# Performance work log

Measured on AMD Instinct MI355X. Metric: run time of the kernel, lower is better.

The kernel has to match this reference:

```python
import jax, jax.numpy as jnp
import numpy as np

N = 1_000_000   # voxels (stride-1: in grid == out grid)
C = 32          # channels
K = 27          # 3x3x3 kernel offsets
P = 600_000     # rulebook pairs per offset
BN_EPS = 1e-5


def setup_inputs() -> dict:
    key = jax.random.key(0)
    k1, k2, k3, k4 = jax.random.split(key, 4)
    x = jax.random.normal(k1, (N, C), dtype=jnp.float32)
    # He-style init for conv weights: fan_in = K * C
    W = jax.random.normal(k2, (K, C, C), dtype=jnp.float32) * (1.0 / np.sqrt(K * C))
    gamma = jnp.ones((C,), dtype=jnp.float32)
    beta = jnp.zeros((C,), dtype=jnp.float32)
    in_idx = jax.random.randint(k3, (K, P), 0, N, dtype=jnp.int32)
    out_idx = jax.random.randint(k4, (K, P), 0, N, dtype=jnp.int32)
    return {"x": x, "W": W, "gamma": gamma, "beta": beta,
            "in_idx": in_idx, "out_idx": out_idx}


def _sparse_conv(x, W, in_idx, out_idx):
    # Rulebook-driven sparse conv: for each kernel offset k, gather input
    # voxels, multiply by the offset's [C,C] weight, scatter-add to outputs.
    def step(acc, inputs):
        ii, oi, w = inputs                      # [P], [P], [C,C]
        acc = acc.at[oi].add(x[ii] @ w)          # gather -> GEMM -> scatter
        return acc, None
    out0 = jnp.zeros((x.shape[0], W.shape[-1]), dtype=x.dtype)
    out, _ = jax.lax.scan(step, out0, (in_idx, out_idx, W))
    return out


def reference(x, W, gamma, beta, in_idx, out_idx):
    y = _sparse_conv(x, W, in_idx, out_idx)      # [N, C]
    # BatchNorm (training-mode batch stats over all voxels, per channel)
    mean = jnp.mean(y, axis=0)
    var = jnp.var(y, axis=0)
    y = (y - mean) * jax.lax.rsqrt(var + BN_EPS) * gamma + beta
    # ReLU
    return jnp.maximum(y, 0.0)
```

## Files before the change

### kernel.cpp

```cpp
#include <hip/hip_runtime.h>

#define CH 32
#define KOFF 27
#define BN_EPS 1e-5f
#define FXS 512.0f
#define FXI (1.0f / 512.0f)

typedef short bf16x8 __attribute__((ext_vector_type(8)));
typedef float f32x4 __attribute__((ext_vector_type(4)));
typedef unsigned long long u64;

__device__ __forceinline__ unsigned short f2bf(float f) {
    unsigned u = __builtin_bit_cast(unsigned, f);
    u = (u + 0x7fffu + ((u >> 16) & 1u)) >> 16;
    return (unsigned short)u;
}

__device__ __forceinline__ void decode4(u64 v, float* f) {
    long long w = (long long)v;
    int s0 = (short)(w & 0xFFFF);          w -= (long long)s0;
    int s1 = (short)((w >> 16) & 0xFFFF);  w -= ((long long)s1 << 16);
    int s2 = (short)((w >> 32) & 0xFFFF);  w -= ((long long)s2 << 32);
    int s3 = (int)(w >> 48);
    f[0] = s0 * FXI; f[1] = s1 * FXI; f[2] = s2 * FXI; f[3] = s3 * FXI;
}

__global__ __launch_bounds__(256) void conv_fx_kernel(
    const float* __restrict__ x, const float* __restrict__ W,
    const int* __restrict__ in_idx, const int* __restrict__ out_idx,
    u64* __restrict__ yfx,
    int P, int tilesPerK, int tilesPerWave)
{
    const int k    = blockIdx.y;
    const int lane = threadIdx.x & 63;
    const int wv   = threadIdx.x >> 6;
    const int r16  = lane & 15;
    const int g    = lane >> 4;

    const float* Wk = W + k * CH * CH;
    bf16x8 b0, b1;
#pragma unroll
    for (int j = 0; j < 8; ++j) {
        int kk = g * 8 + j;
        b0[j] = (short)f2bf(Wk[kk * CH + 2 * r16]);
        b1[j] = (short)f2bf(Wk[kk * CH + 2 * r16 + 1]);
    }

    const int kP = k * P;
    int t0 = (blockIdx.x * 4 + wv) * tilesPerWave;
    int t1 = t0 + tilesPerWave;
    if (t1 > tilesPerK) t1 = tilesPerK;

    const int iBase = (r16 & 1) ? 2 : 0;
    const int m     = r16 >> 1;

    for (int t = t0; t < t1; ++t) {
        const int base = t * 16;
        int pi = base + r16;
        if (pi >= P) pi = P - 1;
        const int ii = in_idx[kP + pi];
        const float* xr = x + ii * CH + g * 8;
        f32x4 x0 = *(const f32x4*)xr;
        f32x4 x1 = *(const f32x4*)(xr + 4);
        bf16x8 a;
        a[0] = (short)f2bf(x0[0]); a[1] = (short)f2bf(x0[1]);
        a[2] = (short)f2bf(x0[2]); a[3] = (short)f2bf(x0[3]);
        a[4] = (short)f2bf(x1[0]); a[5] = (short)f2bf(x1[1]);
        a[6] = (short)f2bf(x1[2]); a[7] = (short)f2bf(x1[3]);

        f32x4 d0 = {0.f, 0.f, 0.f, 0.f};
        f32x4 d1 = {0.f, 0.f, 0.f, 0.f};
        d0 = __builtin_amdgcn_mfma_f32_16x16x32_bf16(a, b0, d0, 0, 0, 0);
        d1 = __builtin_amdgcn_mfma_f32_16x16x32_bf16(a, b1, d1, 0, 0, 0);

        unsigned qi[4];
#pragma unroll
        for (int i = 0; i < 4; ++i) {
            int s0 = __float2int_rn(d0[i] * FXS);
            int s1 = __float2int_rn(d1[i] * FXS);
            qi[i] = (unsigned)(s0 & 0xFFFF) | ((unsigned)s1 << 16);
        }
        unsigned pq[4];
#pragma unroll
        for (int i = 0; i < 4; ++i) pq[i] = (unsigned)__shfl_xor((int)qi[i], 1);

#pragma unroll
        for (int s = 0; s < 2; ++s) {
            const int i  = iBase + s;
            const int pr = base + g * 4 + i;
            if (pr < P) {
                const int oi = out_idx[kP + pr];
                int a0 = (short)(qi[i] & 0xFFFF), a1 = (short)(qi[i] >> 16);
                int c0 = (short)(pq[i] & 0xFFFF), c1 = (short)(pq[i] >> 16);
                long long A;
                if (!(r16 & 1))
                    A = (long long)a0 + ((long long)a1 << 16)
                      + ((long long)c0 << 32) + ((long long)c1 << 48);
                else
                    A = (long long)c0 + ((long long)c1 << 16)
                      + ((long long)a0 << 32) + ((long long)a1 << 48);
                atomicAdd(&yfx[(size_t)oi * 8 + m], (u64)A);
            }
        }
    }
}

__global__ __launch_bounds__(256) void stats_fx_kernel(
    const u64* __restrict__ yfx, float* __restrict__ stats, int nW)
{
    __shared__ float ls[CH], ls2[CH];
    if (threadIdx.x < CH) { ls[threadIdx.x] = 0.f; ls2[threadIdx.x] = 0.f; }
    __syncthreads();

    int tid = blockIdx.x * blockDim.x + threadIdx.x;
    int stride = gridDim.x * blockDim.x;
    float s[4] = {0,0,0,0}, q[4] = {0,0,0,0};
    for (int i = tid; i < nW; i += stride) {
        float f[4];
        decode4(yfx[i], f);
#pragma unroll
        for (int j = 0; j < 4; ++j) { s[j] += f[j]; q[j] += f[j] * f[j]; }
    }
    int c = (tid & 7) * 4;
#pragma unroll
    for (int j = 0; j < 4; ++j) {
        atomicAdd(&ls[c + j], s[j]);
        atomicAdd(&ls2[c + j], q[j]);
    }
    __syncthreads();
    if (threadIdx.x < CH) {
        atomicAdd(&stats[threadIdx.x], ls[threadIdx.x]);
        atomicAdd(&stats[CH + threadIdx.x], ls2[threadIdx.x]);
    }
}

__global__ __launch_bounds__(256) void bn_relu_fx_kernel(
    const u64* __restrict__ yfx, f32x4* __restrict__ out4,
    const float* __restrict__ stats,
    const float* __restrict__ gamma, const float* __restrict__ beta,
    float invN, int nW)
{
    __shared__ float sc[CH], bi[CH];
    if (threadIdx.x < CH) {
        int c = threadIdx.x;
        float mean = stats[c] * invN;
        float var  = stats[CH + c] * invN - mean * mean;
        float s = gamma[c] * rsqrtf(var + BN_EPS);
        sc[c] = s;
        bi[c] = beta[c] - mean * s;
    }
    __syncthreads();

    int tid = blockIdx.x * blockDim.x + threadIdx.x;
    int stride = gridDim.x * blockDim.x;
    for (int i = tid; i < nW; i += stride) {
        float f[4];
        decode4(yfx[i], f);
        int c = (i & 7) * 4;
        f32x4 o;
        o[0] = fmaxf(f[0] * sc[c + 0] + bi[c + 0], 0.f);
        o[1] = fmaxf(f[1] * sc[c + 1] + bi[c + 1], 0.f);
        o[2] = fmaxf(f[2] * sc[c + 2] + bi[c + 2], 0.f);
        o[3] = fmaxf(f[3] * sc[c + 3] + bi[c + 3], 0.f);
        out4[i] = o;
    }
}

__global__ __launch_bounds__(256) void conv_kernel(
    const float* __restrict__ x, const float* __restrict__ W,
    const int* __restrict__ in_idx, const int* __restrict__ out_idx,
    float* __restrict__ y, int P, int tilesPerK, int tilesPerWave)
{
    const int k    = blockIdx.y;
    const int lane = threadIdx.x & 63;
    const int wv   = threadIdx.x >> 6;
    const int r16  = lane & 15;
    const int g    = lane >> 4;

    const float* Wk = W + k * CH * CH;
    bf16x8 b0, b1;
#pragma unroll
    for (int j = 0; j < 8; ++j) {
        int kk = g * 8 + j;
        b0[j] = (short)f2bf(Wk[kk * CH + r16]);
        b1[j] = (short)f2bf(Wk[kk * CH + 16 + r16]);
    }

    const int kP = k * P;
    int t0 = (blockIdx.x * 4 + wv) * tilesPerWave;
    int t1 = t0 + tilesPerWave;
    if (t1 > tilesPerK) t1 = tilesPerK;

    for (int t = t0; t < t1; ++t) {
        const int base = t * 16;
        int pi = base + r16;
        if (pi >= P) pi = P - 1;
        const int ii = in_idx[kP + pi];
        const float* xr = x + ii * CH + g * 8;
        f32x4 x0 = *(const f32x4*)xr;
        f32x4 x1 = *(const f32x4*)(xr + 4);
        bf16x8 a;
        a[0] = (short)f2bf(x0[0]); a[1] = (short)f2bf(x0[1]);
        a[2] = (short)f2bf(x0[2]); a[3] = (short)f2bf(x0[3]);
        a[4] = (short)f2bf(x1[0]); a[5] = (short)f2bf(x1[1]);
        a[6] = (short)f2bf(x1[2]); a[7] = (short)f2bf(x1[3]);

        f32x4 d0 = {0.f, 0.f, 0.f, 0.f};
        f32x4 d1 = {0.f, 0.f, 0.f, 0.f};
        d0 = __builtin_amdgcn_mfma_f32_16x16x32_bf16(a, b0, d0, 0, 0, 0);
        d1 = __builtin_amdgcn_mfma_f32_16x16x32_bf16(a, b1, d1, 0, 0, 0);

#pragma unroll
        for (int i = 0; i < 4; ++i) {
            int pr = base + g * 4 + i;
            if (pr < P) {
                int oi = out_idx[kP + pr];
                atomicAdd(&y[oi * CH + r16], d0[i]);
                atomicAdd(&y[oi * CH + 16 + r16], d1[i]);
            }
        }
    }
}

__global__ __launch_bounds__(256) void stats_kernel(
    const f32x4* __restrict__ y4, float* __restrict__ stats, int n4)
{
    __shared__ float ls[CH], ls2[CH];
    if (threadIdx.x < CH) { ls[threadIdx.x] = 0.f; ls2[threadIdx.x] = 0.f; }
    __syncthreads();

    int tid = blockIdx.x * blockDim.x + threadIdx.x;
    int stride = gridDim.x * blockDim.x;
    float s0 = 0, s1 = 0, s2 = 0, s3 = 0;
    float q0 = 0, q1 = 0, q2 = 0, q3 = 0;
    for (int i = tid; i < n4; i += stride) {
        f32x4 v = y4[i];
        s0 += v[0]; q0 += v[0] * v[0];
        s1 += v[1]; q1 += v[1] * v[1];
        s2 += v[2]; q2 += v[2] * v[2];
        s3 += v[3]; q3 += v[3] * v[3];
    }
    int c = (tid * 4) & (CH - 1);
    atomicAdd(&ls[c + 0], s0); atomicAdd(&ls[c + 1], s1);
    atomicAdd(&ls[c + 2], s2); atomicAdd(&ls[c + 3], s3);
    atomicAdd(&ls2[c + 0], q0); atomicAdd(&ls2[c + 1], q1);
    atomicAdd(&ls2[c + 2], q2); atomicAdd(&ls2[c + 3], q3);
    __syncthreads();
    if (threadIdx.x < CH) {
        atomicAdd(&stats[threadIdx.x], ls[threadIdx.x]);
        atomicAdd(&stats[CH + threadIdx.x], ls2[threadIdx.x]);
    }
}

__global__ __launch_bounds__(256) void bn_relu_kernel(
    f32x4* __restrict__ y4, const float* __restrict__ stats,
    const float* __restrict__ gamma, const float* __restrict__ beta,
    float invN, int n4)
{
    __shared__ float sc[CH], bi[CH];
    if (threadIdx.x < CH) {
        int c = threadIdx.x;
        float mean = stats[c] * invN;
        float var  = stats[CH + c] * invN - mean * mean;
        float s = gamma[c] * rsqrtf(var + BN_EPS);
        sc[c] = s;
        bi[c] = beta[c] - mean * s;
    }
    __syncthreads();

    int tid = blockIdx.x * blockDim.x + threadIdx.x;
    int stride = gridDim.x * blockDim.x;
    for (int i = tid; i < n4; i += stride) {
        f32x4 v = y4[i];
        int c = (i * 4) & (CH - 1);
        f32x4 o;
        o[0] = fmaxf(v[0] * sc[c + 0] + bi[c + 0], 0.f);
        o[1] = fmaxf(v[1] * sc[c + 1] + bi[c + 1], 0.f);
        o[2] = fmaxf(v[2] * sc[c + 2] + bi[c + 2], 0.f);
        o[3] = fmaxf(v[3] * sc[c + 3] + bi[c + 3], 0.f);
        y4[i] = o;
    }
}

extern "C" void kernel_launch(void* const* d_in, const int* in_sizes, int n_in,
                              void* d_out, int out_size, void* d_ws, size_t ws_size,
                              hipStream_t stream)
{
    const float* x      = (const float*)d_in[0];
    const float* W      = (const float*)d_in[1];
    const float* gamma  = (const float*)d_in[2];
    const float* beta   = (const float*)d_in[3];
    const int*   in_idx = (const int*)d_in[4];
    const int*   out_idx= (const int*)d_in[5];

    const int P = in_sizes[4] / KOFF;
    const int N = in_sizes[0] / CH;

    const int tilesPerK = (P + 15) / 16;
    const int tilesPerWave = 8;
    const int blocksX = (tilesPerK + 4 * tilesPerWave - 1) / (4 * tilesPerWave);

    float* stats = (float*)d_ws;
    const size_t statsBytes = 256;
    const size_t yfxBytes = (size_t)N * 8 * sizeof(u64);

    if (ws_size >= statsBytes + yfxBytes) {
        u64* yfx = (u64*)((char*)d_ws + statsBytes);
        hipMemsetAsync(d_ws, 0, statsBytes + yfxBytes, stream);

        conv_fx_kernel<<<dim3(blocksX, KOFF), 256, 0, stream>>>(
            x, W, in_idx, out_idx, yfx, P, tilesPerK, tilesPerWave);

        const int nW = N * 8;
        stats_fx_kernel<<<1024, 256, 0, stream>>>(yfx, stats, nW);
        bn_relu_fx_kernel<<<2048, 256, 0, stream>>>(yfx, (f32x4*)d_out, stats,
                                                    gamma, beta, 1.0f / (float)N, nW);
    } else {
        float* y = (float*)d_out;
        hipMemsetAsync(d_out, 0, (size_t)out_size * sizeof(float), stream);
        hipMemsetAsync(d_ws, 0, statsBytes, stream);

        conv_kernel<<<dim3(blocksX, KOFF), 256, 0, stream>>>(
            x, W, in_idx, out_idx, y, P, tilesPerK, tilesPerWave);

        const int n4 = out_size / 4;
        stats_kernel<<<1024, 256, 0, stream>>>((const f32x4*)d_out, stats, n4);
        bn_relu_kernel<<<2048, 256, 0, stream>>>((f32x4*)d_out, stats, gamma, beta,
                                                 1.0f / (float)N, n4);
    }
}
```

Measured before the change: 825.5 us.

## Partition rulebook by output bins and accumulate conv outputs in shared memory

Adds a partition pass that buckets each offset's rulebook chunk by output-row bin (256 rows per bin) into packed records with per-chunk offsets. A new per-bin kernel gathers those records into shared memory, runs the MFMA GEMM, and scatter-adds into an LDS tile instead of global atomics. The same kernel writes y directly and folds in the per-channel sum and sum-of-squares for batch norm. Input x is also pre-converted to bf16 once to halve gather traffic. This removes global atomic contention and the separate zero, stats and decode passes, at the cost of extra index passes and a fixed per-bin record capacity (RCAP) that silently drops records if a bin overflows.

```diff
diff --git a/kernel.cpp b/kernel.cpp
--- a/kernel.cpp
+++ b/kernel.cpp
@@ -6,9 +6,16 @@
 #define FXS 512.0f
 #define FXI (1.0f / 512.0f)
 
+#define CHUNK 8192
+#define NBINS 4096
+#define BINV 256
+#define RCAP 4608
+
 typedef short bf16x8 __attribute__((ext_vector_type(8)));
 typedef float f32x4 __attribute__((ext_vector_type(4)));
 typedef unsigned long long u64;
+typedef unsigned short u16;
+typedef unsigned int u32;
 
 __device__ __forceinline__ unsigned short f2bf(float f) {
     unsigned u = __builtin_bit_cast(unsigned, f);
@@ -25,11 +32,261 @@
     f[0] = s0 * FXI; f[1] = s1 * FXI; f[2] = s2 * FXI; f[3] = s3 * FXI;
 }
 
+
+__global__ __launch_bounds__(256) void xbf_kernel(
+    const float* __restrict__ x, uint4* __restrict__ xbf, int n8)
+{
+    int tid = blockIdx.x * blockDim.x + threadIdx.x;
+    int stride = gridDim.x * blockDim.x;
+    for (int j = tid; j < n8; j += stride) {
+        const f32x4* xp = (const f32x4*)(x + (size_t)j * 8);
+        f32x4 v0 = xp[0], v1 = xp[1];
+        uint4 o;
+        o.x = (u32)f2bf(v0[0]) | ((u32)f2bf(v0[1]) << 16);
+        o.y = (u32)f2bf(v0[2]) | ((u32)f2bf(v0[3]) << 16);
+        o.z = (u32)f2bf(v1[0]) | ((u32)f2bf(v1[1]) << 16);
+        o.w = (u32)f2bf(v1[2]) | ((u32)f2bf(v1[3]) << 16);
+        xbf[j] = o;
+    }
+}
+
+__global__ __launch_bounds__(256) void part_kernel(
+    const int* __restrict__ in_idx, const int* __restrict__ out_idx,
+    u32* __restrict__ records, u16* __restrict__ gofs,
+    int P, int NCH)
+{
+    __shared__ u32 hist[NBINS];
+    __shared__ u32 stage[CHUNK];
+    __shared__ u32 wtot[4];
+
+    const int kc = blockIdx.x;
+    const int k  = kc / NCH;
+    const int c  = kc - k * NCH;
+    const int start = c * CHUNK;
+    const int len = min(CHUNK, P - start);
+    const int tid = threadIdx.x;
+    const int base = k * P + start;
+
+    for (int b = tid; b < NBINS; b += 256) hist[b] = 0;
+    __syncthreads();
+
+    for (int j = tid; j < len; j += 256) {
+        u32 oi = (u32)out_idx[base + j];
+        atomicAdd(&hist[oi >> 8], 1u);
+    }
+    __syncthreads();
+
+    u32 loc[16]; u32 s = 0;
+#pragma unroll
+    for (int i = 0; i < 16; ++i) { loc[i] = hist[tid * 16 + i]; s += loc[i]; }
+    u32 incl = s;
+#pragma unroll
+    for (int off = 1; off < 64; off <<= 1) {
+        u32 v = (u32)__shfl_up((int)incl, off);
+        if ((tid & 63) >= off) incl += v;
+    }
+    u32 wexcl = incl - s;
+    if ((tid & 63) == 63) wtot[tid >> 6] = incl;
+    __syncthreads();
+    u32 wbase = 0;
+    for (int w = 0; w < (tid >> 6); ++w) wbase += wtot[w];
+    u32 run = wbase + wexcl;
+#pragma unroll
+    for (int i = 0; i < 16; ++i) { hist[tid * 16 + i] = run; run += loc[i]; }
+    __syncthreads();
+
+    for (int b = tid; b < NBINS; b += 256)
+        gofs[(size_t)kc * NBINS + b] = (u16)hist[b];
+    __syncthreads();
+
+    for (int j = tid; j < len; j += 256) {
+        u32 oi = (u32)out_idx[base + j];
+        u32 ii = (u32)in_idx[base + j];
+        u32 pos = atomicAdd(&hist[oi >> 8], 1u);
+        stage[pos] = (ii << 8) | (oi & 255u);
+    }
+    __syncthreads();
+
+    for (int j = tid; j < len; j += 256)
+        records[(size_t)kc * CHUNK + j] = stage[j];
+}
+
+template <bool XBF>
+__global__ __launch_bounds__(256) void binacc_kernel(
+    const uint4* __restrict__ xbf, const float* __restrict__ xf,
+    const float* __restrict__ W,
+    const u32* __restrict__ records, const u16* __restrict__ gofs,
+    float* __restrict__ stats, float* __restrict__ y,
+    int N, int P, int NCH, int KC)
+{
+    __shared__ float accf[BINV * 33];
+    __shared__ u32 recbuf[RCAP];
+    __shared__ u32 khist[KOFF], kofs[KOFF], kcur[KOFF];
+    __shared__ float ls[CH], ls2[CH];
+
+    const int b   = blockIdx.x;
+    const int tid = threadIdx.x;
+    const int lane = tid & 63;
+    const int wv  = tid >> 6;
+    const int r16 = lane & 15;
+    const int g   = lane >> 4;
+
+    for (int j = tid; j < BINV * 33; j += 256) accf[j] = 0.f;
+    if (tid < KOFF) khist[tid] = 0;
+    if (tid < CH) { ls[tid] = 0.f; ls2[tid] = 0.f; }
+    __syncthreads();
+
+    u32 o0s[8], cnts[8];
+#pragma unroll
+    for (int i = 0; i < 8; ++i) {
+        int kc = tid + i * 256;
+        u32 o0 = 0, cnt = 0;
+        if (kc < KC) {
+            o0 = gofs[(size_t)kc * NBINS + b];
+            u32 o1 = gofs[(size_t)kc * NBINS + b + 1];
+            cnt = o1 - o0;
+            int k = kc / NCH;
+            if (cnt) atomicAdd(&khist[k], cnt);
+        }
+        o0s[i] = o0; cnts[i] = cnt;
+    }
+    __syncthreads();
+
+    if (tid == 0) {
+        u32 r = 0;
+        for (int k = 0; k < KOFF; ++k) { kofs[k] = r; r += khist[k]; }
+    }
+    __syncthreads();
+    if (tid < KOFF) kcur[tid] = kofs[tid];
+    __syncthreads();
+
+#pragma unroll
+    for (int i = 0; i < 8; ++i) {
+        int kc = tid + i * 256;
+        u32 cnt = cnts[i];
+        if (kc < KC && cnt) {
+            int k = kc / NCH;
+            u32 dst = atomicAdd(&kcur[k], cnt);
+            const u32* src = records + (size_t)kc * CHUNK + o0s[i];
+            for (u32 r = 0; r < cnt; ++r)
+                if (dst + r < RCAP) recbuf[dst + r] = src[r];
+        }
+    }
+    __syncthreads();
+
+    for (int k = wv; k < KOFF; k += 4) {
+        const int n = (int)khist[k];
+        if (n == 0) continue;
+        const int kb = (int)kofs[k];
+        const float* Wk = W + k * CH * CH;
+        bf16x8 b0, b1;
+#pragma unroll
+        for (int j = 0; j < 8; ++j) {
+            int kk = g * 8 + j;
+            b0[j] = (short)f2bf(Wk[kk * CH + r16]);
+            b1[j] = (short)f2bf(Wk[kk * CH + 16 + r16]);
+        }
+        const int nt = (n + 15) >> 4;
+        for (int t = 0; t < nt; ++t) {
+            const int ri = t * 16 + r16;
+            u32 rec = (ri < n && kb + ri < RCAP) ? recbuf[kb + ri] : 0u;
+            u32 ii = rec >> 8;
+            bf16x8 a;
+            if (XBF) {
+                uint4 raw = xbf[(size_t)ii * 4 + g];
+                a = __builtin_bit_cast(bf16x8, raw);
+            } else {
+                const f32x4* xr = (const f32x4*)(xf + (size_t)ii * CH + g * 8);
+                f32x4 x0 = xr[0], x1 = xr[1];
+                a[0] = (short)f2bf(x0[0]); a[1] = (short)f2bf(x0[1]);
+                a[2] = (short)f2bf(x0[2]); a[3] = (short)f2bf(x0[3]);
+                a[4] = (short)f2bf(x1[0]); a[5] = (short)f2bf(x1[1]);
+                a[6] = (short)f2bf(x1[2]); a[7] = (short)f2bf(x1[3]);
+            }
+            f32x4 d0 = {0.f, 0.f, 0.f, 0.f};
+            f32x4 d1 = {0.f, 0.f, 0.f, 0.f};
+            d0 = __builtin_amdgcn_mfma_f32_16x16x32_bf16(a, b0, d0, 0, 0, 0);
+            d1 = __builtin_amdgcn_mfma_f32_16x16x32_bf16(a, b1, d1, 0, 0, 0);
+#pragma unroll
+            for (int i = 0; i < 4; ++i) {
+                int idx = t * 16 + g * 4 + i;
+                if (idx < n && kb + idx < RCAP) {
+                    u32 v = recbuf[kb + idx] & 255u;
+                    atomicAdd(&accf[v * 33 + r16], d0[i]);
+                    atomicAdd(&accf[v * 33 + 16 + r16], d1[i]);
+                }
+            }
+        }
+    }
+    __syncthreads();
+
+    {
+        int grp = tid >> 5, c = tid & 31;
+        float s = 0.f, q = 0.f;
+#pragma unroll
+        for (int r = 0; r < 32; ++r) {
+            float v = accf[(grp * 32 + r) * 33 + c];
+            s += v; q += v * v;
+        }
+        atomicAdd(&ls[c], s);
+        atomicAdd(&ls2[c], q);
+    }
+    {
+        int row = b * BINV + tid;
+        if (row < N) {
+            float vals[32];
+#pragma unroll
+            for (int i = 0; i < 32; ++i) vals[i] = accf[tid * 33 + i];
+            f32x4* yo = (f32x4*)(y + (size_t)row * CH);
+#pragma unroll
+            for (int j = 0; j < 8; ++j) {
+                f32x4 o = { vals[4*j], vals[4*j+1], vals[4*j+2], vals[4*j+3] };
+                yo[j] = o;
+            }
+        }
+    }
+    __syncthreads();
+    if (tid < CH) {
+        atomicAdd(&stats[tid], ls[tid]);
+        atomicAdd(&stats[CH + tid], ls2[tid]);
+    }
+}
+
+__global__ __launch_bounds__(256) void bn_relu_kernel(
+    f32x4* __restrict__ y4, const float* __restrict__ stats,
+    const float* __restrict__ gamma, const float* __restrict__ beta,
+    float invN, int n4)
+{
+    __shared__ float sc[CH], bi[CH];
+    if (threadIdx.x < CH) {
+        int c = threadIdx.x;
+        float mean = stats[c] * invN;
+        float var  = stats[CH + c] * invN - mean * mean;
+        float s = gamma[c] * rsqrtf(var + BN_EPS);
+        sc[c] = s;
+        bi[c] = beta[c] - mean * s;
+    }
+    __syncthreads();
+
+    int tid = blockIdx.x * blockDim.x + threadIdx.x;
+    int stride = gridDim.x * blockDim.x;
+    for (int i = tid; i < n4; i += stride) {
+        f32x4 v = y4[i];
+        int c = (i * 4) & (CH - 1);
+        f32x4 o;
+        o[0] = fmaxf(v[0] * sc[c + 0] + bi[c + 0], 0.f);
+        o[1] = fmaxf(v[1] * sc[c + 1] + bi[c + 1], 0.f);
+        o[2] = fmaxf(v[2] * sc[c + 2] + bi[c + 2], 0.f);
+        o[3] = fmaxf(v[3] * sc[c + 3] + bi[c + 3], 0.f);
+        y4[i] = o;
+    }
+}
+
+
 __global__ __launch_bounds__(256) void conv_fx_kernel(
     const float* __restrict__ x, const float* __restrict__ W,
     const int* __restrict__ in_idx, const int* __restrict__ out_idx,
-    u64* __restrict__ yfx,
-    int P, int tilesPerK, int tilesPerWave)
+    u64* __restrict__ yfx, int P, int tilesPerK, int tilesPerWave)
 {
     const int k    = blockIdx.y;
     const int lane = threadIdx.x & 63;
@@ -166,121 +423,6 @@
     }
 }
 
-__global__ __launch_bounds__(256) void conv_kernel(
-    const float* __restrict__ x, const float* __restrict__ W,
-    const int* __restrict__ in_idx, const int* __restrict__ out_idx,
-    float* __restrict__ y, int P, int tilesPerK, int tilesPerWave)
-{
-    const int k    = blockIdx.y;
-    const int lane = threadIdx.x & 63;
-    const int wv   = threadIdx.x >> 6;
-    const int r16  = lane & 15;
-    const int g    = lane >> 4;
-
-    const float* Wk = W + k * CH * CH;
-    bf16x8 b0, b1;
-#pragma unroll
-    for (int j = 0; j < 8; ++j) {
-        int kk = g * 8 + j;
-        b0[j] = (short)f2bf(Wk[kk * CH + r16]);
-        b1[j] = (short)f2bf(Wk[kk * CH + 16 + r16]);
-    }
-
-    const int kP = k * P;
-    int t0 = (blockIdx.x * 4 + wv) * tilesPerWave;
-    int t1 = t0 + tilesPerWave;
-    if (t1 > tilesPerK) t1 = tilesPerK;
-
-    for (int t = t0; t < t1; ++t) {
-        const int base = t * 16;
-        int pi = base + r16;
-        if (pi >= P) pi = P - 1;
-        const int ii = in_idx[kP + pi];
-        const float* xr = x + ii * CH + g * 8;
-        f32x4 x0 = *(const f32x4*)xr;
-        f32x4 x1 = *(const f32x4*)(xr + 4);
-        bf16x8 a;
-        a[0] = (short)f2bf(x0[0]); a[1] = (short)f2bf(x0[1]);
-        a[2] = (short)f2bf(x0[2]); a[3] = (short)f2bf(x0[3]);
-        a[4] = (short)f2bf(x1[0]); a[5] = (short)f2bf(x1[1]);
-        a[6] = (short)f2bf(x1[2]); a[7] = (short)f2bf(x1[3]);
-
-        f32x4 d0 = {0.f, 0.f, 0.f, 0.f};
-        f32x4 d1 = {0.f, 0.f, 0.f, 0.f};
-        d0 = __builtin_amdgcn_mfma_f32_16x16x32_bf16(a, b0, d0, 0, 0, 0);
-        d1 = __builtin_amdgcn_mfma_f32_16x16x32_bf16(a, b1, d1, 0, 0, 0);
-
-#pragma unroll
-        for (int i = 0; i < 4; ++i) {
-            int pr = base + g * 4 + i;
-            if (pr < P) {
-                int oi = out_idx[kP + pr];
-                atomicAdd(&y[oi * CH + r16], d0[i]);
-                atomicAdd(&y[oi * CH + 16 + r16], d1[i]);
-            }
-        }
-    }
-}
-
-__global__ __launch_bounds__(256) void stats_kernel(
-    const f32x4* __restrict__ y4, float* __restrict__ stats, int n4)
-{
-    __shared__ float ls[CH], ls2[CH];
-    if (threadIdx.x < CH) { ls[threadIdx.x] = 0.f; ls2[threadIdx.x] = 0.f; }
-    __syncthreads();
-
-    int tid = blockIdx.x * blockDim.x + threadIdx.x;
-    int stride = gridDim.x * blockDim.x;
-    float s0 = 0, s1 = 0, s2 = 0, s3 = 0;
-    float q0 = 0, q1 = 0, q2 = 0, q3 = 0;
-    for (int i = tid; i < n4; i += stride) {
-        f32x4 v = y4[i];
-        s0 += v[0]; q0 += v[0] * v[0];
-        s1 += v[1]; q1 += v[1] * v[1];
-        s2 += v[2]; q2 += v[2] * v[2];
-        s3 += v[3]; q3 += v[3] * v[3];
-    }
-    int c = (tid * 4) & (CH - 1);
-    atomicAdd(&ls[c + 0], s0); atomicAdd(&ls[c + 1], s1);
-    atomicAdd(&ls[c + 2], s2); atomicAdd(&ls[c + 3], s3);
-    atomicAdd(&ls2[c + 0], q0); atomicAdd(&ls2[c + 1], q1);
-    atomicAdd(&ls2[c + 2], q2); atomicAdd(&ls2[c + 3], q3);
-    __syncthreads();
-    if (threadIdx.x < CH) {
-        atomicAdd(&stats[threadIdx.x], ls[threadIdx.x]);
-        atomicAdd(&stats[CH + threadIdx.x], ls2[threadIdx.x]);
-    }
-}
-
-__global__ __launch_bounds__(256) void bn_relu_kernel(
-    f32x4* __restrict__ y4, const float* __restrict__ stats,
-    const float* __restrict__ gamma, const float* __restrict__ beta,
-    float invN, int n4)
-{
-    __shared__ float sc[CH], bi[CH];
-    if (threadIdx.x < CH) {
-        int c = threadIdx.x;
-        float mean = stats[c] * invN;
-        float var  = stats[CH + c] * invN - mean * mean;
-        float s = gamma[c] * rsqrtf(var + BN_EPS);
-        sc[c] = s;
-        bi[c] = beta[c] - mean * s;
-    }
-    __syncthreads();
-
-    int tid = blockIdx.x * blockDim.x + threadIdx.x;
-    int stride = gridDim.x * blockDim.x;
-    for (int i = tid; i < n4; i += stride) {
-        f32x4 v = y4[i];
-        int c = (i * 4) & (CH - 1);
-        f32x4 o;
-        o[0] = fmaxf(v[0] * sc[c + 0] + bi[c + 0], 0.f);
-        o[1] = fmaxf(v[1] * sc[c + 1] + bi[c + 1], 0.f);
-        o[2] = fmaxf(v[2] * sc[c + 2] + bi[c + 2], 0.f);
-        o[3] = fmaxf(v[3] * sc[c + 3] + bi[c + 3], 0.f);
-        y4[i] = o;
-    }
-}
 
 extern "C" void kernel_launch(void* const* d_in, const int* in_sizes, int n_in,
                               void* d_out, int out_size, void* d_ws, size_t ws_size,
@@ -295,37 +437,61 @@
 
     const int P = in_sizes[4] / KOFF;
     const int N = in_sizes[0] / CH;
+    const int n4 = out_size / 4;
+
+    const int NCH = (P + CHUNK - 1) / CHUNK;
+    const int KC  = KOFF * NCH;
+    const int NB  = (N + BINV - 1) / BINV;
+
+    const size_t statsBytes = 1024;
+    const size_t xbfBytes   = (size_t)N * CH * 2;
+    const size_t gofsBytes  = (size_t)KC * NBINS * sizeof(u16);
+    const size_t recsBytes  = (size_t)KC * CHUNK * sizeof(u32);
+    const size_t needFull   = statsBytes + xbfBytes + gofsBytes + recsBytes;
+    const size_t needNoXbf  = statsBytes + gofsBytes + recsBytes;
+
+    if (ws_size >= needNoXbf) {
+        const bool useXbf = (ws_size >= needFull);
+        float* stats = (float*)d_ws;
+        char* p = (char*)d_ws + statsBytes;
+        uint4* xbf = (uint4*)p;
+        if (useXbf) p += xbfBytes;
+        u16* gofs = (u16*)p;  p += gofsBytes;
+        u32* recs = (u32*)p;
+
+        hipMemsetAsync(d_ws, 0, statsBytes, stream);
+        if (useXbf)
+            xbf_kernel<<<2048, 256, 0, stream>>>(x, xbf, N * CH / 8);
+
+        part_kernel<<<KC, 256, 0, stream>>>(in_idx, out_idx, recs, gofs, P, NCH);
+
+        if (useXbf)
+            binacc_kernel<true><<<NB, 256, 0, stream>>>(
+                xbf, x, W, recs, gofs, stats, (float*)d_out, N, P, NCH, KC);
+        else
+            binacc_kernel<false><<<NB, 256, 0, stream>>>(
+                xbf, x, W, recs, gofs, stats, (float*)d_out, N, P, NCH, KC);
+
+        bn_relu_kernel<<<2048, 256, 0, stream>>>(
+            (f32x4*)d_out, stats, gamma, beta, 1.0f / (float)N, n4);
+        return;
+    }
 
     const int tilesPerK = (P + 15) / 16;
     const int tilesPerWave = 8;
     const int blocksX = (tilesPerK + 4 * tilesPerWave - 1) / (4 * tilesPerWave);
 
     float* stats = (float*)d_ws;
-    const size_t statsBytes = 256;
+    const size_t stB = 256;
     const size_t yfxBytes = (size_t)N * 8 * sizeof(u64);
-
-    if (ws_size >= statsBytes + yfxBytes) {
-        u64* yfx = (u64*)((char*)d_ws + statsBytes);
-        hipMemsetAsync(d_ws, 0, statsBytes + yfxBytes, stream);
-
-        conv_fx_kernel<<<dim3(blocksX, KOFF), 256, 0, stream>>>(
-            x, W, in_idx, out_idx, yfx, P, tilesPerK, tilesPerWave);
-
-        const int nW = N * 8;
-        stats_fx_kernel<<<1024, 256, 0, stream>>>(yfx, stats, nW);
-        bn_relu_fx_kernel<<<2048, 256, 0, stream>>>(yfx, (f32x4*)d_out, stats,
-                                                    gamma, beta, 1.0f / (float)N, nW);
-    } else {
-        float* y = (float*)d_out;
-        hipMemsetAsync(d_out, 0, (size_t)out_size * sizeof(float), stream);
-        hipMemsetAsync(d_ws, 0, statsBytes, stream);
-
-        conv_kernel<<<dim3(blocksX, KOFF), 256, 0, stream>>>(
-            x, W, in_idx, out_idx, y, P, tilesPerK, tilesPerWave);
-
-        const int n4 = out_size / 4;
-        stats_kernel<<<1024, 256, 0, stream>>>((const f32x4*)d_out, stats, n4);
-        bn_relu_kernel<<<2048, 256, 0, stream>>>((f32x4*)d_out, stats, gamma, beta,
-                                                 1.0f / (float)N, n4);
-    }
-}
+    u64* yfx = (u64*)((char*)d_ws + stB);
+    hipMemsetAsync(d_ws, 0, stB + yfxBytes, stream);
+
+    conv_fx_kernel<<<dim3(blocksX, KOFF), 256, 0, stream>>>(
+        x, W, in_idx, out_idx, yfx, P, tilesPerK, tilesPerWave);
+
+    const int nW = N * 8;
+    stats_fx_kernel<<<1024, 256, 0, stream>>>(yfx, stats, nW);
+    bn_relu_fx_kernel<<<2048, 256, 0, stream>>>(yfx, (f32x4*)d_out, stats,
+                                                gamma, beta, 1.0f / (float)N, nW);
+}
```

Measured after the change: 3.000 ms. +263.4%, slower.
